# Optimization experiments

Measured on AMD Instinct MI355X. Metric: run time of the kernel, lower is better.

Reference implementation:

```python
import jax, jax.numpy as jnp
import numpy as np
import math

N_ITEMS = 200000
N_USERS = 100000
D = 128
E_II = 3200000
E_UI = 1600000


def spmm(src, dst, val, x, n_rows):
    # out[i] = sum_{e: dst[e]==i} val[e] * x[src[e]]
    return jax.ops.segment_sum(val[:, None] * x[src], dst, num_segments=n_rows)


def leaky_relu(x):
    return jnp.where(x >= 0, x, 0.2 * x)


def setup_inputs() -> dict:
    key = jax.random.key(0)
    ks = jax.random.split(key, 16)
    d = {}
    d["b"] = 2
    d["items_emb"] = jax.random.normal(ks[0], (N_ITEMS, D), dtype=jnp.float32) * 0.1
    for i, rel in enumerate(["p2p_in", "p2p_out", "e2p_in"]):
        d[f"src_{rel}"] = jax.random.randint(ks[1 + 3 * i], (E_II,), 0, N_ITEMS, dtype=jnp.int32)
        d[f"dst_{rel}"] = jax.random.randint(ks[2 + 3 * i], (E_II,), 0, N_ITEMS, dtype=jnp.int32)
        d[f"val_{rel}"] = jax.random.uniform(ks[3 + 3 * i], (E_II,), dtype=jnp.float32) / 16.0
    d["src_ui"] = jax.random.randint(ks[10], (E_UI,), 0, N_ITEMS, dtype=jnp.int32)
    d["dst_ui"] = jax.random.randint(ks[11], (E_UI,), 0, N_USERS, dtype=jnp.int32)
    d["val_ui"] = jax.random.uniform(ks[12], (E_UI,), dtype=jnp.float32) / 16.0
    s = 1.0 / math.sqrt(D)
    d["I_p2p_in"] = jax.random.normal(ks[13], (D, D), dtype=jnp.float32) * s
    d["I_p2p_out"] = jax.random.normal(ks[14], (D, D), dtype=jnp.float32) * s
    d["I_e2p_in"] = jax.random.normal(ks[15], (D, D), dtype=jnp.float32) * s
    return d


def reference(b, items_emb, src_p2p_in, dst_p2p_in, val_p2p_in,
              src_p2p_out, dst_p2p_out, val_p2p_out,
              src_e2p_in, dst_e2p_in, val_e2p_in,
              src_ui, dst_ui, val_ui,
              I_p2p_in, I_p2p_out, I_e2p_in):
    assert b == 2  # static branch, matches torch `if b == 2`
    x = items_emb
    n = x.shape[0]
    inv_sqrt_d = 1.0 / math.sqrt(x.shape[1])

    # multi-relation sparse aggregation (torch.spmm)
    nb_in = spmm(src_p2p_in, dst_p2p_in, val_p2p_in, x, n)
    nb_out = spmm(src_p2p_out, dst_p2p_out, val_p2p_out, x, n)
    nb_e2p = spmm(src_e2p_in, dst_e2p_in, val_e2p_in, x, n)

    # gated attention over relations
    h_in = leaky_relu((x * nb_in) @ I_p2p_in)
    h_out = leaky_relu((x * nb_out) @ I_p2p_out)
    h_e2p = leaky_relu((x * nb_e2p) @ I_e2p_in)
    s_in = jnp.sum(h_in, axis=1) * inv_sqrt_d
    s_out = jnp.sum(h_out, axis=1) * inv_sqrt_d
    s_e2p = jnp.sum(h_e2p, axis=1) * inv_sqrt_d
    score = jax.nn.softmax(jnp.stack((s_in, s_out, s_e2p), axis=1), axis=1)  # [n,3]
    neighbor = (nb_in * score[:, 0:1]
                + nb_out * score[:, 1:2]
                + nb_e2p * score[:, 2:3])

    # uiGNN: user embeddings from item embeddings
    u_emb = spmm(src_ui, dst_ui, val_ui, x, N_USERS)
    return (u_emb, neighbor)
```

## Files before the change

kernel.cpp:

```cpp
#include <hip/hip_runtime.h>

#define D 128
#define N_ITEMS 200000
#define N_USERS 100000
#define TI 64
#define ST 132

#define INV_SQRT_D 0.088388347648318447f

__global__ __launch_bounds__(256) void hist_kernel(
    const int* __restrict__ dst, unsigned* __restrict__ counts, int E)
{
    int e = blockIdx.x * 256 + threadIdx.x;
    if (e < E) atomicAdd(&counts[dst[e]], 1u);
}

__global__ __launch_bounds__(256) void scan1_kernel(
    const unsigned* __restrict__ counts, unsigned* __restrict__ offsets,
    unsigned* __restrict__ blocksums, int n)
{
    __shared__ unsigned s[256];
    int tid = threadIdx.x;
    int i = blockIdx.x * 256 + tid;
    unsigned v = (i < n) ? counts[i] : 0u;
    s[tid] = v; __syncthreads();
    #pragma unroll
    for (int off = 1; off < 256; off <<= 1) {
        unsigned t = (tid >= off) ? s[tid - off] : 0u;
        __syncthreads();
        s[tid] += t;
        __syncthreads();
    }
    if (i < n) offsets[i] = s[tid] - v;
    if (tid == 255) blocksums[blockIdx.x] = s[255];
}

__global__ __launch_bounds__(1024) void scan2_kernel(
    unsigned* __restrict__ blocksums, int nb)
{
    __shared__ unsigned s[1024];
    int tid = threadIdx.x;
    unsigned v = (tid < nb) ? blocksums[tid] : 0u;
    s[tid] = v; __syncthreads();
    #pragma unroll
    for (int off = 1; off < 1024; off <<= 1) {
        unsigned t = (tid >= off) ? s[tid - off] : 0u;
        __syncthreads();
        s[tid] += t;
        __syncthreads();
    }
    if (tid < nb) blocksums[tid] = s[tid] - v;
}

__global__ __launch_bounds__(256) void scan3_kernel(
    unsigned* __restrict__ offsets, unsigned* __restrict__ cursor,
    const unsigned* __restrict__ blocksums, int n, unsigned Etot)
{
    int i = blockIdx.x * 256 + threadIdx.x;
    if (i < n) {
        unsigned o = offsets[i] + blocksums[blockIdx.x];
        offsets[i] = o;
        cursor[i] = o;
    }
    if (i == 0) offsets[n] = Etot;
}

__global__ __launch_bounds__(256) void scatter_kernel(
    const int* __restrict__ src, const int* __restrict__ dst,
    const float* __restrict__ val, unsigned* __restrict__ cursor,
    int2* __restrict__ pairs, int E)
{
    int e = blockIdx.x * 256 + threadIdx.x;
    if (e >= E) return;
    unsigned pos = atomicAdd(&cursor[dst[e]], 1u);
    pairs[pos] = make_int2(src[e], __float_as_int(val[e]));
}

__global__ __launch_bounds__(256) void gather_spmm_kernel(
    const unsigned* __restrict__ offsets, const int2* __restrict__ pairs,
    const float4* __restrict__ x4, float4* __restrict__ out4, int nrows)
{
    int row = blockIdx.x * 8 + (threadIdx.x >> 5);
    if (row >= nrows) return;
    int lane = threadIdx.x & 31;
    unsigned j = offsets[row], end = offsets[row + 1];
    float4 acc = make_float4(0.f, 0.f, 0.f, 0.f);
    for (; j + 2 <= end; j += 2) {
        int2 p0 = pairs[j];
        int2 p1 = pairs[j + 1];
        float4 a = x4[(size_t)p0.x * 32 + lane];
        float4 b = x4[(size_t)p1.x * 32 + lane];
        float v0 = __int_as_float(p0.y), v1 = __int_as_float(p1.y);
        acc.x = fmaf(v0, a.x, acc.x); acc.y = fmaf(v0, a.y, acc.y);
        acc.z = fmaf(v0, a.z, acc.z); acc.w = fmaf(v0, a.w, acc.w);
        acc.x = fmaf(v1, b.x, acc.x); acc.y = fmaf(v1, b.y, acc.y);
        acc.z = fmaf(v1, b.z, acc.z); acc.w = fmaf(v1, b.w, acc.w);
    }
    if (j < end) {
        int2 p0 = pairs[j];
        float4 a = x4[(size_t)p0.x * 32 + lane];
        float v0 = __int_as_float(p0.y);
        acc.x = fmaf(v0, a.x, acc.x); acc.y = fmaf(v0, a.y, acc.y);
        acc.z = fmaf(v0, a.z, acc.z); acc.w = fmaf(v0, a.w, acc.w);
    }
    out4[(size_t)row * 32 + lane] = acc;
}

__global__ __launch_bounds__(256, 4) void score_combine_kernel(
    const float4* __restrict__ x4,
    float4* __restrict__ nb0,
    const float4* __restrict__ nb1, const float4* __restrict__ nb2,
    const float4* __restrict__ I0, const float4* __restrict__ I1,
    const float4* __restrict__ I2)
{
    __shared__ __align__(16) float Tt[TI * ST];
    __shared__ float Wl[TI * 3];
    const int tid = threadIdx.x;
    const int jg = tid & 15;
    const int ig = tid >> 4;
    const int i0 = ig << 2;
    const int itemBase = blockIdx.x * TI;

    const float4* nbs[3] = {(const float4*)nb0, nb1, nb2};
    const float4* Is[3]  = {I0, I1, I2};
    float sreg[3][4];

    #pragma unroll
    for (int rel = 0; rel < 3; ++rel) {
        __syncthreads();
        const float4* nbp = nbs[rel];
        #pragma unroll
        for (int it = 0; it < 8; ++it) {
            int f4 = it * 256 + tid;
            int il = f4 >> 5, dd4 = f4 & 31;
            size_t g = (size_t)(itemBase + il) * 32 + dd4;
            float4 a = x4[g], b = nbp[g];
            float4 p;
            p.x = a.x * b.x; p.y = a.y * b.y;
            p.z = a.z * b.z; p.w = a.w * b.w;
            *(float4*)&Tt[il * ST + (dd4 << 2)] = p;
        }
        __syncthreads();

        const float4* Ip = Is[rel];
        float acc[4][8];
        #pragma unroll
        for (int a = 0; a < 4; ++a)
            #pragma unroll
            for (int b = 0; b < 8; ++b) acc[a][b] = 0.f;

        const float* t0 = &Tt[(i0 + 0) * ST];
        const float* t1 = &Tt[(i0 + 1) * ST];
        const float* t2 = &Tt[(i0 + 2) * ST];
        const float* t3 = &Tt[(i0 + 3) * ST];

        #pragma unroll 4
        for (int k = 0; k < D; ++k) {
            float4 iv0 = Ip[k * 32 + (jg << 1)];
            float4 iv1 = Ip[k * 32 + (jg << 1) + 1];
            float tv0 = t0[k], tv1 = t1[k], tv2 = t2[k], tv3 = t3[k];
            acc[0][0] = fmaf(tv0, iv0.x, acc[0][0]);
            acc[0][1] = fmaf(tv0, iv0.y, acc[0][1]);
            acc[0][2] = fmaf(tv0, iv0.z, acc[0][2]);
            acc[0][3] = fmaf(tv0, iv0.w, acc[0][3]);
            acc[0][4] = fmaf(tv0, iv1.x, acc[0][4]);
            acc[0][5] = fmaf(tv0, iv1.y, acc[0][5]);
            acc[0][6] = fmaf(tv0, iv1.z, acc[0][6]);
            acc[0][7] = fmaf(tv0, iv1.w, acc[0][7]);
            acc[1][0] = fmaf(tv1, iv0.x, acc[1][0]);
            acc[1][1] = fmaf(tv1, iv0.y, acc[1][1]);
            acc[1][2] = fmaf(tv1, iv0.z, acc[1][2]);
            acc[1][3] = fmaf(tv1, iv0.w, acc[1][3]);
            acc[1][4] = fmaf(tv1, iv1.x, acc[1][4]);
            acc[1][5] = fmaf(tv1, iv1.y, acc[1][5]);
            acc[1][6] = fmaf(tv1, iv1.z, acc[1][6]);
            acc[1][7] = fmaf(tv1, iv1.w, acc[1][7]);
            acc[2][0] = fmaf(tv2, iv0.x, acc[2][0]);
            acc[2][1] = fmaf(tv2, iv0.y, acc[2][1]);
            acc[2][2] = fmaf(tv2, iv0.z, acc[2][2]);
            acc[2][3] = fmaf(tv2, iv0.w, acc[2][3]);
            acc[2][4] = fmaf(tv2, iv1.x, acc[2][4]);
            acc[2][5] = fmaf(tv2, iv1.y, acc[2][5]);
            acc[2][6] = fmaf(tv2, iv1.z, acc[2][6]);
            acc[2][7] = fmaf(tv2, iv1.w, acc[2][7]);
            acc[3][0] = fmaf(tv3, iv0.x, acc[3][0]);
            acc[3][1] = fmaf(tv3, iv0.y, acc[3][1]);
            acc[3][2] = fmaf(tv3, iv0.z, acc[3][2]);
            acc[3][3] = fmaf(tv3, iv0.w, acc[3][3]);
            acc[3][4] = fmaf(tv3, iv1.x, acc[3][4]);
            acc[3][5] = fmaf(tv3, iv1.y, acc[3][5]);
            acc[3][6] = fmaf(tv3, iv1.z, acc[3][6]);
            acc[3][7] = fmaf(tv3, iv1.w, acc[3][7]);
        }

        #pragma unroll
        for (int a = 0; a < 4; ++a) {
            float s = 0.f;
            #pragma unroll
            for (int b = 0; b < 8; ++b) {
                float h = acc[a][b];
                s += (h >= 0.f) ? h : 0.2f * h;
            }
            #pragma unroll
            for (int off = 8; off; off >>= 1)
                s += __shfl_down(s, off, 16);
            sreg[rel][a] = s * INV_SQRT_D;
        }
    }

    if (jg == 0) {
        #pragma unroll
        for (int a = 0; a < 4; ++a) {
            float s0 = sreg[0][a], s1 = sreg[1][a], s2 = sreg[2][a];
            float m = fmaxf(s0, fmaxf(s1, s2));
            float e0 = expf(s0 - m), e1 = expf(s1 - m), e2 = expf(s2 - m);
            float inv = 1.f / (e0 + e1 + e2);
            int il = i0 + a;
            Wl[il * 3 + 0] = e0 * inv;
            Wl[il * 3 + 1] = e1 * inv;
            Wl[il * 3 + 2] = e2 * inv;
        }
    }
    __syncthreads();

    #pragma unroll
    for (int it = 0; it < 8; ++it) {
        int f4 = it * 256 + tid;
        int il = f4 >> 5, dd4 = f4 & 31;
        size_t g = (size_t)(itemBase + il) * 32 + dd4;
        float w0 = Wl[il * 3 + 0], w1 = Wl[il * 3 + 1], w2 = Wl[il * 3 + 2];
        float4 a = nb0[g], b = nb1[g], c = nb2[g];
        float4 r;
        r.x = fmaf(w0, a.x, fmaf(w1, b.x, w2 * c.x));
        r.y = fmaf(w0, a.y, fmaf(w1, b.y, w2 * c.y));
        r.z = fmaf(w0, a.z, fmaf(w1, b.z, w2 * c.z));
        r.w = fmaf(w0, a.w, fmaf(w1, b.w, w2 * c.w));
        nb0[g] = r;
    }
}

extern "C" void kernel_launch(void* const* d_in, const int* in_sizes, int n_in,
                              void* d_out, int out_size, void* d_ws, size_t ws_size,
                              hipStream_t stream) {
    const float* x       = (const float*)d_in[1];
    const int*   src0    = (const int*)d_in[2];
    const int*   dst0    = (const int*)d_in[3];
    const float* val0    = (const float*)d_in[4];
    const int*   src1    = (const int*)d_in[5];
    const int*   dst1    = (const int*)d_in[6];
    const float* val1    = (const float*)d_in[7];
    const int*   src2    = (const int*)d_in[8];
    const int*   dst2    = (const int*)d_in[9];
    const float* val2    = (const float*)d_in[10];
    const int*   src_ui  = (const int*)d_in[11];
    const int*   dst_ui  = (const int*)d_in[12];
    const float* val_ui  = (const float*)d_in[13];
    const float* I0      = (const float*)d_in[14];
    const float* I1      = (const float*)d_in[15];
    const float* I2      = (const float*)d_in[16];

    const int E_ii = in_sizes[2];
    const int E_ui = in_sizes[11];

    float* u_emb = (float*)d_out;
    float* nb0   = (float*)d_out + (size_t)N_USERS * D;

    float*    nb1       = (float*)d_ws;
    float*    nb2       = nb1 + (size_t)N_ITEMS * D;
    unsigned* cc        = (unsigned*)(nb2 + (size_t)N_ITEMS * D);
    unsigned* offsets   = cc + N_ITEMS;
    unsigned* blocksums = offsets + N_ITEMS + 1;
    uintptr_t pu        = ((uintptr_t)(blocksums + 1024) + 15) & ~(uintptr_t)15;
    int2*     pairs_ui  = (int2*)pu;
    int2*     pairs_ii  = (int2*)d_out;

    auto build_and_gather = [&](const int* src, const int* dst, const float* val,
                                int E, int nrows, int2* pairs, float* out) {
        hipMemsetAsync(cc, 0, (size_t)nrows * sizeof(unsigned), stream);
        int gE = (E + 255) / 256;
        int gN = (nrows + 255) / 256;
        hist_kernel<<<gE, 256, 0, stream>>>(dst, cc, E);
        scan1_kernel<<<gN, 256, 0, stream>>>(cc, offsets, blocksums, nrows);
        scan2_kernel<<<1, 1024, 0, stream>>>(blocksums, gN);
        scan3_kernel<<<gN, 256, 0, stream>>>(offsets, cc, blocksums, nrows, (unsigned)E);
        scatter_kernel<<<gE, 256, 0, stream>>>(src, dst, val, cc, pairs, E);
        gather_spmm_kernel<<<(nrows + 7) / 8, 256, 0, stream>>>(
            offsets, pairs, (const float4*)x, (float4*)out, nrows);
    };

    build_and_gather(src0, dst0, val0, E_ii, N_ITEMS, pairs_ii, nb0);
    build_and_gather(src1, dst1, val1, E_ii, N_ITEMS, pairs_ii, nb1);
    build_and_gather(src2, dst2, val2, E_ii, N_ITEMS, pairs_ii, nb2);

    score_combine_kernel<<<N_ITEMS / TI, 256, 0, stream>>>(
        (const float4*)x, (float4*)nb0, (const float4*)nb1, (const float4*)nb2,
        (const float4*)I0, (const float4*)I1, (const float4*)I2);

    build_and_gather(src_ui, dst_ui, val_ui, E_ui, N_USERS, pairs_ui, u_emb);
}
```

Before: 2.889 ms.

## Restructure score GEMM with transposed LDS tile and wave-uniform weight loads

```diff
diff --git a/kernel.cpp b/kernel.cpp
--- a/kernel.cpp
+++ b/kernel.cpp
@@ -4,7 +4,6 @@
 #define N_ITEMS 200000
 #define N_USERS 100000
 #define TI 64
-#define ST 132
 
 #define INV_SQRT_D 0.088388347648318447f
 
@@ -110,123 +109,95 @@
     const float4* __restrict__ x4,
     float4* __restrict__ nb0,
     const float4* __restrict__ nb1, const float4* __restrict__ nb2,
-    const float4* __restrict__ I0, const float4* __restrict__ I1,
-    const float4* __restrict__ I2)
-{
-    __shared__ __align__(16) float Tt[TI * ST];
+    const float* __restrict__ I0, const float* __restrict__ I1,
+    const float* __restrict__ I2)
+{
+    __shared__ float Tt[D * 65];
+    __shared__ float Sred[3 * 4 * 64];
     __shared__ float Wl[TI * 3];
-    const int tid = threadIdx.x;
-    const int jg = tid & 15;
-    const int ig = tid >> 4;
-    const int i0 = ig << 2;
+
+    const int tid  = threadIdx.x;
+    const int lane = tid & 63;
+    const int wv   = __builtin_amdgcn_readfirstlane(tid >> 6);
+    const int ilo  = tid >> 5;
+    const int dd4  = tid & 31;
     const int itemBase = blockIdx.x * TI;
 
+    float4 xr[8];
+    #pragma unroll
+    for (int it = 0; it < 8; ++it) {
+        int il = it * 8 + ilo;
+        xr[it] = x4[(size_t)(itemBase + il) * 32 + dd4];
+    }
+
     const float4* nbs[3] = {(const float4*)nb0, nb1, nb2};
-    const float4* Is[3]  = {I0, I1, I2};
-    float sreg[3][4];
-
-    #pragma unroll
+    const float*  Is[3]  = {I0, I1, I2};
+
     for (int rel = 0; rel < 3; ++rel) {
         __syncthreads();
         const float4* nbp = nbs[rel];
         #pragma unroll
         for (int it = 0; it < 8; ++it) {
-            int f4 = it * 256 + tid;
-            int il = f4 >> 5, dd4 = f4 & 31;
-            size_t g = (size_t)(itemBase + il) * 32 + dd4;
-            float4 a = x4[g], b = nbp[g];
-            float4 p;
-            p.x = a.x * b.x; p.y = a.y * b.y;
-            p.z = a.z * b.z; p.w = a.w * b.w;
-            *(float4*)&Tt[il * ST + (dd4 << 2)] = p;
+            int il = it * 8 + ilo;
+            float4 b = nbp[(size_t)(itemBase + il) * 32 + dd4];
+            float4 a = xr[it];
+            int base = (dd4 * 4) * 65 + il;
+            Tt[base]       = a.x * b.x;
+            Tt[base + 65]  = a.y * b.y;
+            Tt[base + 130] = a.z * b.z;
+            Tt[base + 195] = a.w * b.w;
         }
         __syncthreads();
 
-        const float4* Ip = Is[rel];
-        float acc[4][8];
-        #pragma unroll
-        for (int a = 0; a < 4; ++a)
+        const float4* Iw4 = (const float4*)Is[rel] + wv * 8;
+        float4 acc[8];
+        #pragma unroll
+        for (int c = 0; c < 8; ++c) acc[c] = make_float4(0.f, 0.f, 0.f, 0.f);
+
+        #pragma unroll 2
+        for (int k = 0; k < D; ++k) {
+            float tv = Tt[k * 65 + lane];
             #pragma unroll
-            for (int b = 0; b < 8; ++b) acc[a][b] = 0.f;
-
-        const float* t0 = &Tt[(i0 + 0) * ST];
-        const float* t1 = &Tt[(i0 + 1) * ST];
-        const float* t2 = &Tt[(i0 + 2) * ST];
-        const float* t3 = &Tt[(i0 + 3) * ST];
-
-        #pragma unroll 4
-        for (int k = 0; k < D; ++k) {
-            float4 iv0 = Ip[k * 32 + (jg << 1)];
-            float4 iv1 = Ip[k * 32 + (jg << 1) + 1];
-            float tv0 = t0[k], tv1 = t1[k], tv2 = t2[k], tv3 = t3[k];
-            acc[0][0] = fmaf(tv0, iv0.x, acc[0][0]);
-            acc[0][1] = fmaf(tv0, iv0.y, acc[0][1]);
-            acc[0][2] = fmaf(tv0, iv0.z, acc[0][2]);
-            acc[0][3] = fmaf(tv0, iv0.w, acc[0][3]);
-            acc[0][4] = fmaf(tv0, iv1.x, acc[0][4]);
-            acc[0][5] = fmaf(tv0, iv1.y, acc[0][5]);
-            acc[0][6] = fmaf(tv0, iv1.z, acc[0][6]);
-            acc[0][7] = fmaf(tv0, iv1.w, acc[0][7]);
-            acc[1][0] = fmaf(tv1, iv0.x, acc[1][0]);
-            acc[1][1] = fmaf(tv1, iv0.y, acc[1][1]);
-            acc[1][2] = fmaf(tv1, iv0.z, acc[1][2]);
-            acc[1][3] = fmaf(tv1, iv0.w, acc[1][3]);
-            acc[1][4] = fmaf(tv1, iv1.x, acc[1][4]);
-            acc[1][5] = fmaf(tv1, iv1.y, acc[1][5]);
-            acc[1][6] = fmaf(tv1, iv1.z, acc[1][6]);
-            acc[1][7] = fmaf(tv1, iv1.w, acc[1][7]);
-            acc[2][0] = fmaf(tv2, iv0.x, acc[2][0]);
-            acc[2][1] = fmaf(tv2, iv0.y, acc[2][1]);
-            acc[2][2] = fmaf(tv2, iv0.z, acc[2][2]);
-            acc[2][3] = fmaf(tv2, iv0.w, acc[2][3]);
-            acc[2][4] = fmaf(tv2, iv1.x, acc[2][4]);
-            acc[2][5] = fmaf(tv2, iv1.y, acc[2][5]);
-            acc[2][6] = fmaf(tv2, iv1.z, acc[2][6]);
-            acc[2][7] = fmaf(tv2, iv1.w, acc[2][7]);
-            acc[3][0] = fmaf(tv3, iv0.x, acc[3][0]);
-            acc[3][1] = fmaf(tv3, iv0.y, acc[3][1]);
-            acc[3][2] = fmaf(tv3, iv0.z, acc[3][2]);
-            acc[3][3] = fmaf(tv3, iv0.w, acc[3][3]);
-            acc[3][4] = fmaf(tv3, iv1.x, acc[3][4]);
-            acc[3][5] = fmaf(tv3, iv1.y, acc[3][5]);
-            acc[3][6] = fmaf(tv3, iv1.z, acc[3][6]);
-            acc[3][7] = fmaf(tv3, iv1.w, acc[3][7]);
+            for (int c = 0; c < 8; ++c) {
+                float4 iv = Iw4[k * 32 + c];
+                acc[c].x = fmaf(tv, iv.x, acc[c].x);
+                acc[c].y = fmaf(tv, iv.y, acc[c].y);
+                acc[c].z = fmaf(tv, iv.z, acc[c].z);
+                acc[c].w = fmaf(tv, iv.w, acc[c].w);
+            }
         }
 
-        #pragma unroll
-        for (int a = 0; a < 4; ++a) {
-            float s = 0.f;
-            #pragma unroll
-            for (int b = 0; b < 8; ++b) {
-                float h = acc[a][b];
-                s += (h >= 0.f) ? h : 0.2f * h;
-            }
-            #pragma unroll
-            for (int off = 8; off; off >>= 1)
-                s += __shfl_down(s, off, 16);
-            sreg[rel][a] = s * INV_SQRT_D;
+        float s = 0.f;
+        #pragma unroll
+        for (int c = 0; c < 8; ++c) {
+            s += fmaxf(acc[c].x, 0.2f * acc[c].x);
+            s += fmaxf(acc[c].y, 0.2f * acc[c].y);
+            s += fmaxf(acc[c].z, 0.2f * acc[c].z);
+            s += fmaxf(acc[c].w, 0.2f * acc[c].w);
         }
-    }
-
-    if (jg == 0) {
-        #pragma unroll
-        for (int a = 0; a < 4; ++a) {
-            float s0 = sreg[0][a], s1 = sreg[1][a], s2 = sreg[2][a];
-            float m = fmaxf(s0, fmaxf(s1, s2));
-            float e0 = expf(s0 - m), e1 = expf(s1 - m), e2 = expf(s2 - m);
-            float inv = 1.f / (e0 + e1 + e2);
-            int il = i0 + a;
-            Wl[il * 3 + 0] = e0 * inv;
-            Wl[il * 3 + 1] = e1 * inv;
-            Wl[il * 3 + 2] = e2 * inv;
-        }
+        Sred[rel * 256 + wv * 64 + lane] = s;
     }
     __syncthreads();
 
+    if (tid < TI) {
+        float sr[3];
+        #pragma unroll
+        for (int r = 0; r < 3; ++r)
+            sr[r] = (Sred[r * 256 + tid] + Sred[r * 256 + 64 + tid] +
+                     Sred[r * 256 + 128 + tid] + Sred[r * 256 + 192 + tid])
+                    * INV_SQRT_D;
+        float m = fmaxf(sr[0], fmaxf(sr[1], sr[2]));
+        float e0 = expf(sr[0] - m), e1 = expf(sr[1] - m), e2 = expf(sr[2] - m);
+        float inv = 1.f / (e0 + e1 + e2);
+        Wl[tid * 3 + 0] = e0 * inv;
+        Wl[tid * 3 + 1] = e1 * inv;
+        Wl[tid * 3 + 2] = e2 * inv;
+    }
+    __syncthreads();
+
     #pragma unroll
     for (int it = 0; it < 8; ++it) {
-        int f4 = it * 256 + tid;
-        int il = f4 >> 5, dd4 = f4 & 31;
+        int il = it * 8 + ilo;
         size_t g = (size_t)(itemBase + il) * 32 + dd4;
         float w0 = Wl[il * 3 + 0], w1 = Wl[il * 3 + 1], w2 = Wl[il * 3 + 2];
         float4 a = nb0[g], b = nb1[g], c = nb2[g];
@@ -294,7 +265,7 @@
 
     score_combine_kernel<<<N_ITEMS / TI, 256, 0, stream>>>(
         (const float4*)x, (float4*)nb0, (const float4*)nb1, (const float4*)nb2,
-        (const float4*)I0, (const float4*)I1, (const float4*)I2);
+        I0, I1, I2);
 
     build_and_gather(src_ui, dst_ui, val_ui, E_ui, N_USERS, pairs_ui, u_emb);
 }
```

Result: faster. 2.558 ms (-11.5%).
